# Kernel tuning notes

Hardware: AMD Instinct MI355X
Metric: run time of the kernel (lower is better)

The kernel has to match this reference:

```python
import jax, jax.numpy as jnp
import numpy as np
import math

D_MODEL = 512
N_HEADS = 8
D_FF = 2048
E_LAYERS = 2
ENC_IN = 3
MA_K = 25            # moving_avg kernel size
FACTOR = 1
B, L_CYC, CDL = 16, 20, 128
SEQ = L_CYC * CDL    # 2560
TOP_K = int(FACTOR * math.log(SEQ))  # 7
OUTPUT_NUM = 1


def moving_avg(x, k=MA_K):
    # x: [B,S,D]; replicate-pad ends by (k-1)//2, stride-1 mean pool -> length S
    p = (k - 1) // 2
    xp = jnp.concatenate([jnp.repeat(x[:, :1], p, axis=1), x, jnp.repeat(x[:, -1:], p, axis=1)], axis=1)
    c = jnp.cumsum(xp, axis=1)
    c = jnp.concatenate([jnp.zeros_like(c[:, :1]), c], axis=1)
    return (c[:, k:] - c[:, :-k]) / k


def token_embed(x, W):
    # x: [B,S,C], W: [D_MODEL, C, 3]; Conv1d k=3, circular padding, no bias
    xc = jnp.pad(x.transpose(0, 2, 1), ((0, 0), (0, 0), (1, 1)), mode='wrap')
    y = jax.lax.conv_general_dilated(xc, W, (1,), 'VALID', dimension_numbers=('NCH', 'OIH', 'NCH'))
    return y.transpose(0, 2, 1)  # [B,S,D]


def autocorrelation(q, k, v):
    # q,k,v: [B,S,H,E]; FFT autocorrelation + top-k time-delay aggregation (inference path)
    B_, S, H, E = q.shape
    qf = jnp.fft.rfft(q.transpose(0, 2, 3, 1), axis=-1)      # [B,H,E,F]
    kf = jnp.fft.rfft(k.transpose(0, 2, 3, 1), axis=-1)
    corr = jnp.fft.irfft(qf * jnp.conj(kf), n=S, axis=-1)    # [B,H,E,S]
    vals = v.transpose(0, 2, 3, 1)                           # [B,H,E,S]
    mean_corr = corr.mean(axis=(1, 2))                       # [B,S]
    weights, delay = jax.lax.top_k(mean_corr, TOP_K)         # [B,K]
    w = jax.nn.softmax(weights, axis=-1)

    def agg_one(v_b, d_b, w_b):
        # roll by -delay == gather values at index (t + delay) mod S
        out = jnp.zeros_like(v_b)
        for i in range(TOP_K):
            out = out + jnp.roll(v_b, -d_b[i], axis=-1) * w_b[i]
        return out

    V = jax.vmap(agg_one)(vals, delay, w)                    # [B,H,E,S]
    return V.transpose(0, 3, 1, 2)                           # [B,S,H,E]


def my_layernorm(x, g, b):
    # LayerNorm over last dim, then subtract the per-series (time) mean
    mu = x.mean(-1, keepdims=True)
    var = ((x - mu) ** 2).mean(-1, keepdims=True)
    xh = (x - mu) / jnp.sqrt(var + 1e-5) * g + b
    return xh - xh.mean(axis=1, keepdims=True)


def encoder_layer(x, Wq, bq, Wk, bk, Wv, bv, Wo, bo, Wc1, Wc2):
    B_, S, D = x.shape
    H, E = N_HEADS, D // N_HEADS
    q = (x @ Wq + bq).reshape(B_, S, H, E)
    k = (x @ Wk + bk).reshape(B_, S, H, E)
    v = (x @ Wv + bv).reshape(B_, S, H, E)
    att = autocorrelation(q, k, v).reshape(B_, S, D)
    x = x + (att @ Wo + bo)
    x = x - moving_avg(x)                                    # series_decomp1: residual part
    y = jax.nn.gelu(x @ Wc1, approximate=False) @ Wc2        # 1x1 convs, no bias
    z = x + y
    return z - moving_avg(z)                                 # series_decomp2


def setup_inputs() -> dict:
    key = jax.random.key(0)
    ks = jax.random.split(key, 12)
    s = 0.02
    rn = lambda k, shape: jax.random.normal(k, shape, dtype=jnp.float32) * s
    return {
        'cycle_curve_data': jax.random.normal(ks[0], (B, L_CYC, ENC_IN, CDL), dtype=jnp.float32),
        'curve_attn_mask': jnp.ones((B, L_CYC), dtype=jnp.float32),
        'W_emb': rn(ks[1], (D_MODEL, ENC_IN, 3)),
        'Wq': rn(ks[2], (E_LAYERS, D_MODEL, D_MODEL)),
        'bq': jnp.zeros((E_LAYERS, D_MODEL), jnp.float32),
        'Wk': rn(ks[3], (E_LAYERS, D_MODEL, D_MODEL)),
        'bk': jnp.zeros((E_LAYERS, D_MODEL), jnp.float32),
        'Wv': rn(ks[4], (E_LAYERS, D_MODEL, D_MODEL)),
        'bv': jnp.zeros((E_LAYERS, D_MODEL), jnp.float32),
        'Wo': rn(ks[5], (E_LAYERS, D_MODEL, D_MODEL)),
        'bo': jnp.zeros((E_LAYERS, D_MODEL), jnp.float32),
        'Wc1': rn(ks[6], (E_LAYERS, D_MODEL, D_FF)),
        'Wc2': rn(ks[7], (E_LAYERS, D_FF, D_MODEL)),
        'gamma': jnp.ones((D_MODEL,), jnp.float32),
        'beta': jnp.zeros((D_MODEL,), jnp.float32),
        'Wp': rn(ks[8], (D_MODEL * SEQ, OUTPUT_NUM)),
        'bp': jnp.zeros((OUTPUT_NUM,), jnp.float32),
    }


def reference(cycle_curve_data, curve_attn_mask, W_emb, Wq, bq, Wk, bk, Wv, bv, Wo, bo, Wc1, Wc2, gamma, beta, Wp, bp):
    mask = curve_attn_mask[:, :, None, None]                 # [B,L,1,1]
    x = jnp.where(mask == 0, 0.0, cycle_curve_data)          # zero masked cycles
    Bn = x.shape[0]
    x = x.transpose(0, 1, 3, 2).reshape(Bn, SEQ, ENC_IN)     # [B, L*CDL, NV]
    h = token_embed(x, W_emb)                                # DataEmbedding_wo_pos (x_mark=None, dropout=0)
    for l in range(E_LAYERS):
        h = encoder_layer(h, Wq[l], bq[l], Wk[l], bk[l], Wv[l], bv[l], Wo[l], bo[l], Wc1[l], Wc2[l])
    h = my_layernorm(h, gamma, beta)
    out = jax.nn.gelu(h, approximate=False)
    emb = out.reshape(Bn, -1)
    return emb @ Wp + bp                                     # [B, OUTPUT_NUM]
```

## Files before the change

### kernel.cpp

```cpp
#include <hip/hip_runtime.h>
#include <math.h>

#define BATCH 16
#define L_CYC 20
#define CDL 128
#define SEQ 2560
#define ENC_IN 3
#define DMODEL 512
#define DFF 2048
#define NLAYERS 2
#define TOPK 7
#define MROWS (BATCH*SEQ)
#define SD ((size_t)BATCH * SEQ * DMODEL)
#define FFN_CHUNK 20480
#define CHUNK_D 256
#define DGRP 8
#define FFT_NT 512

typedef short bf16x8 __attribute__((ext_vector_type(8)));
typedef float f32x4 __attribute__((ext_vector_type(4)));

__device__ __forceinline__ float gelu_f(float x) {
    float z = x * 0.70710678118654752f;
    float az = fabsf(z);
    float t = __builtin_amdgcn_rcpf(1.0f + 0.3275911f * az);
    float poly = t * (0.254829592f + t * (-0.284496736f + t * (1.421413741f
               + t * (-1.453152027f + t * 1.061405429f))));
    float e = __expf(-az * az);
    float erfv = 1.0f - poly * e;
    erfv = copysignf(erfv, z);
    return 0.5f * x * (1.0f + erfv);
}
__device__ __forceinline__ unsigned short f2bf(float f) {
    unsigned int u = __float_as_uint(f);
    u += 0x7fff + ((u >> 16) & 1);
    return (unsigned short)(u >> 16);
}
__device__ __forceinline__ float bf2f(unsigned short h) {
    return __uint_as_float(((unsigned int)h) << 16);
}
__device__ __forceinline__ void xcd_map(int p, int G, int& g, int& n) {
    int a = p >> 3;
    n = a % G;
    g = (a / G) * 8 + (p & 7);
}
__device__ __forceinline__ void gload16(const unsigned short* g, unsigned short* l) {
    typedef unsigned int u32;
    __builtin_amdgcn_global_load_lds(
        (const __attribute__((address_space(1))) u32*)g,
        (__attribute__((address_space(3))) u32*)l, 16, 0, 0);
}

__global__ __launch_bounds__(256) void embed_kernel(
    const float* __restrict__ data, const float* __restrict__ mask,
    const float* __restrict__ Wemb, float* __restrict__ h,
    unsigned short* __restrict__ hi, unsigned short* __restrict__ lo) {
    __shared__ float xv[2][9];
    int tid = threadIdx.x;
    size_t r0 = (size_t)blockIdx.x * 2;
    if (tid < 18) {
        int lr = tid / 9, k = tid % 9;
        int t = k / 3, c = k % 3;
        size_t r = r0 + lr;
        int s = (int)(r % SEQ);
        int b = (int)(r / SEQ);
        int u = s - 1 + t;
        if (u < 0) u += SEQ;
        if (u >= SEQ) u -= SEQ;
        int cyc = u >> 7, pos = u & 127;
        float mk = mask[b * L_CYC + cyc];
        xv[lr][c * 3 + t] = (mk == 0.f) ? 0.f
            : data[(((size_t)b * L_CYC + cyc) * ENC_IN + c) * CDL + pos];
    }
    __syncthreads();
    int lr = tid >> 7;
    int dm = (tid & 127) * 4;
    size_t idx = (r0 + lr) * DMODEL + dm;
    float a[4];
#pragma unroll
    for (int q = 0; q < 4; q++) {
        float acc = 0.f;
#pragma unroll
        for (int j = 0; j < 9; j++) acc += xv[lr][j] * Wemb[(dm + q) * 9 + j];
        a[q] = acc;
    }
    *(float4*)(h + idx) = make_float4(a[0], a[1], a[2], a[3]);
    ushort4 hv = make_ushort4(f2bf(a[0]), f2bf(a[1]), f2bf(a[2]), f2bf(a[3]));
    *(ushort4*)(hi + idx) = hv;
    ushort4 lv = make_ushort4(f2bf(a[0] - bf2f(hv.x)), f2bf(a[1] - bf2f(hv.y)),
                              f2bf(a[2] - bf2f(hv.z)), f2bf(a[3] - bf2f(hv.w)));
    *(ushort4*)(lo + idx) = lv;
}

__global__ __launch_bounds__(256) void transpose_bf16_kernel(
    const float* __restrict__ W, unsigned short* __restrict__ Wt, int K, int N) {
    __shared__ float t[32][33];
    int n0 = blockIdx.x * 32, k0 = blockIdx.y * 32;
    int c = threadIdx.x & 31, r = threadIdx.x >> 5;
    for (int i = 0; i < 4; i++)
        t[r + i * 8][c] = W[(size_t)(k0 + r + i * 8) * N + n0 + c];
    __syncthreads();
    for (int i = 0; i < 4; i++)
        Wt[(size_t)(n0 + r + i * 8) * K + k0 + c] = f2bf(t[c][r + i * 8]);
}

__global__ __launch_bounds__(256) void transpose_split_stk_kernel(
    const float* __restrict__ W, unsigned short* __restrict__ WtH,
    unsigned short* __restrict__ WtL, int which) {
    __shared__ float t[32][33];
    int n0 = blockIdx.x * 32, k0 = blockIdx.y * 32;
    int c = threadIdx.x & 31, r = threadIdx.x >> 5;
    for (int i = 0; i < 4; i++)
        t[r + i * 8][c] = W[(size_t)(k0 + r + i * 8) * DMODEL + n0 + c];
    __syncthreads();
    for (int i = 0; i < 4; i++) {
        int n = n0 + r + i * 8;
        int row = (n & 255) + ((n >> 8) * 512) + which * 256;
        float v = t[c][r + i * 8];
        unsigned short h = f2bf(v);
        size_t o = (size_t)row * DMODEL + k0 + c;
        WtH[o] = h;
        WtL[o] = f2bf(v - bf2f(h));
    }
}

__global__ void stack_bias_kernel(const float* __restrict__ bq,
                                  const float* __restrict__ bk, float* __restrict__ bstk) {
    int i = blockIdx.x * 256 + threadIdx.x;
    if (i >= 1024) return;
    int c = i >> 9, j = i & 511;
    bstk[i] = (j < 256) ? bq[c * 256 + j] : bk[c * 256 + (j - 256)];
}

__global__ __launch_bounds__(256) void wvo_kernel(
    const float* __restrict__ Wv, const float* __restrict__ Wo,
    float* __restrict__ Wvo) {
    __shared__ float row[DMODEL];
    int k = blockIdx.x;
    int tid = threadIdx.x;
    for (int j = tid; j < DMODEL; j += 256) row[j] = Wv[(size_t)k * DMODEL + j];
    __syncthreads();
    float a0 = 0.f, a1 = 0.f;
    for (int j = 0; j < DMODEL; j++) {
        float wv = row[j];
        a0 += wv * Wo[(size_t)j * DMODEL + tid];
        a1 += wv * Wo[(size_t)j * DMODEL + tid + 256];
    }
    Wvo[(size_t)k * DMODEL + tid] = a0;
    Wvo[(size_t)k * DMODEL + tid + 256] = a1;
}

__global__ void cbias_kernel(const float* __restrict__ bv, const float* __restrict__ Wo,
                             const float* __restrict__ bo, float* __restrict__ cb) {
    int n = blockIdx.x * 256 + threadIdx.x;
    if (n >= DMODEL) return;
    float acc = bo[n];
    for (int j = 0; j < DMODEL; j++) acc += bv[j] * Wo[(size_t)j * DMODEL + n];
    cb[n] = acc;
}

#define BK 64
__global__ __launch_bounds__(256) void gemm_mfma_kernel(
    const unsigned short* __restrict__ A, const unsigned short* __restrict__ Wt,
    const float* __restrict__ bias, const float* res,
    void* Cout, int M, int N, int K, int act, int outMode, int gridN)
{
    __shared__ unsigned short As[128 * 64];
    __shared__ unsigned short Bs[128 * 64];
    int tid = threadIdx.x;
    int wave = tid >> 6, lane = tid & 63;
    int wm = wave & 1, wn = wave >> 1;
    int gblk, nblk;
    xcd_map(blockIdx.x, gridN, gblk, nblk);
    int bm = gblk * 128, bn = nblk * 128;

    int r8 = lane >> 3;
    int swc = ((lane & 7) ^ r8) * 8;
    const unsigned short* Agb = A  + (size_t)(bm + wave * 32 + r8) * K + swc;
    const unsigned short* Bgb = Wt + (size_t)(bn + wave * 32 + r8) * K + swc;
    unsigned short* AsW = As + wave * 32 * 64;
    unsigned short* BsW = Bs + wave * 32 * 64;

    f32x4 acc[4][4] = {};
    int frow = lane & 15;
    int fj = lane >> 4;
    int s7 = frow & 7;

    for (int k0 = 0; k0 < K; k0 += BK) {
        __syncthreads();
#pragma unroll
        for (int i = 0; i < 4; i++) {
            gload16(Agb + (size_t)(i * 8) * K + k0, AsW + i * 8 * 64);
            gload16(Bgb + (size_t)(i * 8) * K + k0, BsW + i * 8 * 64);
        }
        asm volatile("s_waitcnt vmcnt(0)" ::: "memory");
        __syncthreads();
#pragma unroll
        for (int kk = 0; kk < 2; kk++) {
            int c16 = (((kk << 2) | fj) ^ s7) << 3;
            bf16x8 af[4], bfv[4];
#pragma unroll
            for (int mi = 0; mi < 4; mi++)
                af[mi] = *(const bf16x8*)&As[(wm * 64 + mi * 16 + frow) * 64 + c16];
#pragma unroll
            for (int nj = 0; nj < 4; nj++)
                bfv[nj] = *(const bf16x8*)&Bs[(wn * 64 + nj * 16 + frow) * 64 + c16];
#pragma unroll
            for (int mi = 0; mi < 4; mi++)
#pragma unroll
                for (int nj = 0; nj < 4; nj++)
                    acc[mi][nj] = __builtin_amdgcn_mfma_f32_16x16x32_bf16(
                        af[mi], bfv[nj], acc[mi][nj], 0, 0, 0);
        }
    }

    int lrow = (lane >> 4) * 4, lcol = lane & 15;
#pragma unroll
    for (int mi = 0; mi < 4; mi++) {
        int row0 = bm + wm * 64 + mi * 16 + lrow;
#pragma unroll
        for (int nj = 0; nj < 4; nj++) {
            int col = bn + wn * 64 + nj * 16 + lcol;
            float bv = bias ? bias[col] : 0.f;
            f32x4 v = acc[mi][nj];
#pragma unroll
            for (int r = 0; r < 4; r++) {
                int row = row0 + r;
                float x = v[r] + bv;
                if (res) x += res[(size_t)row * N + col];
                if (act == 1) x = gelu_f(x);
                if (outMode == 0) ((float*)Cout)[(size_t)row * N + col] = x;
                else              ((unsigned short*)Cout)[(size_t)row * N + col] = f2bf(x);
            }
        }
    }
}

#define QBK 32
__global__ __launch_bounds__(256) void gemm_qk_split_kernel(
    const unsigned short* __restrict__ Ahi, const unsigned short* __restrict__ Alo,
    const unsigned short* __restrict__ Whi, const unsigned short* __restrict__ Wlo,
    const float* __restrict__ bias, float* __restrict__ Ct, int M, int K, int gridN)
{
    __shared__ unsigned short AsH[128 * 32];
    __shared__ unsigned short AsL[128 * 32];
    __shared__ unsigned short BsH[128 * 32];
    __shared__ unsigned short BsL[128 * 32];
    int tid = threadIdx.x;
    int wave = tid >> 6, lane = tid & 63;
    int wm = wave & 1, wn = wave >> 1;
    int gblk, nblk;
    xcd_map(blockIdx.x, gridN, gblk, nblk);
    int bm = gblk * 128, bn = nblk * 128;

    int lrs = lane >> 2;
    int lk  = (((lane & 3) ^ ((lane >> 3) & 3))) * 8;

    f32x4 acc[4][4] = {};
    int frow = lane & 15;
    int fk = (((lane >> 4) ^ ((frow >> 1) & 3))) * 8;

    for (int k0 = 0; k0 < K; k0 += QBK) {
        __syncthreads();
#pragma unroll
        for (int i = 0; i < 2; i++) {
            int j = wave * 2 + i;
            int row = j * 16 + lrs;
            size_t oa = (size_t)(bm + row) * K + k0 + lk;
            size_t ob = (size_t)(bn + row) * K + k0 + lk;
            gload16(Ahi + oa, AsH + j * 512);
            gload16(Alo + oa, AsL + j * 512);
            gload16(Whi + ob, BsH + j * 512);
            gload16(Wlo + ob, BsL + j * 512);
        }
        asm volatile("s_waitcnt vmcnt(0)" ::: "memory");
        __syncthreads();
        bf16x8 afh[4], afl[4], bfh[4], bfl[4];
#pragma unroll
        for (int mi = 0; mi < 4; mi++) {
            int o = (wm * 64 + mi * 16 + frow) * 32 + fk;
            afh[mi] = *(const bf16x8*)&AsH[o];
            afl[mi] = *(const bf16x8*)&AsL[o];
        }
#pragma unroll
        for (int nj = 0; nj < 4; nj++) {
            int o = (wn * 64 + nj * 16 + frow) * 32 + fk;
            bfh[nj] = *(const bf16x8*)&BsH[o];
            bfl[nj] = *(const bf16x8*)&BsL[o];
        }
#pragma unroll
        for (int mi = 0; mi < 4; mi++)
#pragma unroll
            for (int nj = 0; nj < 4; nj++) {
                acc[mi][nj] = __builtin_amdgcn_mfma_f32_16x16x32_bf16(
                    afh[mi], bfh[nj], acc[mi][nj], 0, 0, 0);
                acc[mi][nj] = __builtin_amdgcn_mfma_f32_16x16x32_bf16(
                    afh[mi], bfl[nj], acc[mi][nj], 0, 0, 0);
                acc[mi][nj] = __builtin_amdgcn_mfma_f32_16x16x32_bf16(
                    afl[mi], bfh[nj], acc[mi][nj], 0, 0, 0);
            }
    }

    int lrow = (lane >> 4) * 4, lcol = lane & 15;
#pragma unroll
    for (int mi = 0; mi < 4; mi++) {
        int row0 = bm + wm * 64 + mi * 16 + lrow;
#pragma unroll
        for (int nj = 0; nj < 4; nj++) {
            int col = bn + wn * 64 + nj * 16 + lcol;
            float bv = bias ? bias[col] : 0.f;
            f32x4 v = acc[mi][nj];
#pragma unroll
            for (int r = 0; r < 4; r++)
                Ct[(size_t)col * M + row0 + r] = v[r] + bv;
        }
    }
}

__device__ __forceinline__ int swz(int a) { return a ^ ((a >> 4) & 15); }

template<int LOGS, int NT>
__device__ __forceinline__ void radix4_stage(const float2* __restrict__ X,
                                             float2* __restrict__ Y,
                                             const float2* __restrict__ w512x,
                                             int tid) {
    const int s = 1 << LOGS;
    for (int t = tid; t < 640; t += NT) {
        int sub = t >> 7, r = t & 127;
        int base = sub << 9;
        int q = r & (s - 1);
        int ps = r - q;
        float2 x0 = X[swz(base + r)];
        float2 x1 = X[swz(base + r + 128)];
        float2 x2 = X[swz(base + r + 256)];
        float2 x3 = X[swz(base + r + 384)];
        float A0r = x0.x + x2.x, A0i = x0.y + x2.y;
        float B0r = x1.x + x3.x, B0i = x1.y + x3.y;
        float A1r = x0.x - x2.x, A1i = x0.y - x2.y;
        float B1r = x1.x - x3.x, B1i = x1.y - x3.y;
        float2 w1 = w512x[ps];
        float w2r = w1.x * w1.x - w1.y * w1.y;
        float w2i = 2.0f * w1.x * w1.y;
        float w3r = w2r * w1.x - w2i * w1.y;
        float w3i = w2r * w1.y + w2i * w1.x;
        float u1r = A1r + B1i, u1i = A1i - B1r;
        float u2r = A0r - B0r, u2i = A0i - B0i;
        float u3r = A1r - B1i, u3i = A1i + B1r;
        int ob = base + q + 4 * ps;
        Y[swz(ob)]         = make_float2(A0r + B0r, A0i + B0i);
        Y[swz(ob + s)]     = make_float2(u1r * w1.x - u1i * w1.y,
                                         u1r * w1.y + u1i * w1.x);
        Y[swz(ob + 2 * s)] = make_float2(u2r * w2r - u2i * w2i,
                                         u2r * w2i + u2i * w2r);
        Y[swz(ob + 3 * s)] = make_float2(u3r * w3r - u3i * w3i,
                                         u3r * w3i + u3i * w3r);
    }
}

template<int NT>
__device__ void fft2560(const float2* x, float2* bufA, float2* bufB,
                        const float2* w512x, const float2* tw, int tid) {
    {
        const float w5r[5] = { 1.f,  0.30901699437494742f, -0.80901699437494742f,
                              -0.80901699437494742f,  0.30901699437494742f };
        const float w5i[5] = { 0.f, -0.95105651629515357f, -0.58778525229247312f,
                               0.58778525229247312f,  0.95105651629515357f };
#pragma unroll
        for (int k1 = 0; k1 < 5; k1++) {
            float ar = 0.f, ai = 0.f;
#pragma unroll
            for (int n1 = 0; n1 < 5; n1++) {
                int m = (n1 * k1) % 5;
                ar += x[n1].x * w5r[m] - x[n1].y * w5i[m];
                ai += x[n1].x * w5i[m] + x[n1].y * w5r[m];
            }
            if (k1 == 0) {
                bufB[swz(tid)] = make_float2(ar, ai);
            } else {
                float2 w = tw[k1 - 1];
                bufB[swz(k1 * 512 + tid)] =
                    make_float2(ar * w.x - ai * w.y, ar * w.y + ai * w.x);
            }
        }
    }
    __syncthreads();
    radix4_stage<0, NT>(bufB, bufA, w512x, tid); __syncthreads();
    radix4_stage<2, NT>(bufA, bufB, w512x, tid); __syncthreads();
    radix4_stage<4, NT>(bufB, bufA, w512x, tid); __syncthreads();
    radix4_stage<6, NT>(bufA, bufB, w512x, tid); __syncthreads();
    for (int t = tid; t < 1280; t += NT) {
        int sub = t >> 8, q = t & 255;
        int base = sub << 9;
        float2 a = bufB[swz(base + q)];
        float2 b = bufB[swz(base + q + 256)];
        bufA[swz(base + q)]       = make_float2(a.x + b.x, a.y + b.y);
        bufA[swz(base + q + 256)] = make_float2(a.x - b.x, a.y - b.y);
    }
    __syncthreads();
}

__global__ __launch_bounds__(FFT_NT) void fft_fwd_kernel(
    const float* __restrict__ qt, const float* __restrict__ kt, float* __restrict__ Z)
{
    __shared__ float2 bufA[SEQ];
    __shared__ float2 bufB[SEQ];
    __shared__ float2 w512x[512];
    int d0 = blockIdx.x * DGRP;
    int b = blockIdx.y;
    int tid = threadIdx.x;
    {
        float sn, cs;
        sincosf(-6.283185307179586f * (float)tid / 512.0f, &sn, &cs);
        w512x[tid] = make_float2(cs, sn);
    }
    float2 tw[4];
#pragma unroll
    for (int k1 = 1; k1 <= 4; k1++) {
        float sn, cs;
        sincosf(-2.4543692606170259e-3f * (float)(k1 * tid), &sn, &cs);
        tw[k1 - 1] = make_float2(cs, sn);
    }
    float accR[5], accI[5];
#pragma unroll
    for (int j = 0; j < 5; j++) { accR[j] = 0.f; accI[j] = 0.f; }

    for (int col = 0; col < DGRP; col++) {
        const float* qcol = qt + (size_t)(d0 + col) * MROWS + (size_t)b * SEQ;
        const float* kcol = kt + (size_t)(d0 + col) * MROWS + (size_t)b * SEQ;
        float2 x[5];
#pragma unroll
        for (int m = 0; m < 5; m++)
            x[m] = make_float2(qcol[m * 512 + tid], kcol[m * 512 + tid]);
        fft2560<FFT_NT>(x, bufA, bufB, w512x, tw, tid);
#pragma unroll
        for (int j = 0; j < 5; j++) {
            int f = tid + FFT_NT * j;
            int fpos = (f % 5) * 512 + (f / 5);
            int g = f ? (SEQ - f) : 0;
            int gpos = (g % 5) * 512 + (g / 5);
            float2 Z1 = bufA[swz(fpos)], Z2 = bufA[swz(gpos)];
            accR[j] += 0.5f * (Z1.x * Z2.y + Z1.y * Z2.x);
            accI[j] += 0.25f * ((Z1.x * Z1.x + Z1.y * Z1.y)
                              - (Z2.x * Z2.x + Z2.y * Z2.y));
        }
    }
#pragma unroll
    for (int j = 0; j < 5; j++) {
        int f = tid + FFT_NT * j;
        int fpos = (f % 5) * 512 + (f / 5);
        atomicAdd(&Z[((size_t)b * SEQ + fpos) * 2 + 0], accR[j]);
        atomicAdd(&Z[((size_t)b * SEQ + fpos) * 2 + 1], accI[j]);
    }
}

__global__ __launch_bounds__(FFT_NT) void fft_inv_kernel(
    const float* __restrict__ Z, float* __restrict__ mc)
{
    __shared__ float2 bufA[SEQ];
    __shared__ float2 bufB[SEQ];
    __shared__ float2 w512x[512];
    int b = blockIdx.x;
    int tid = threadIdx.x;
    {
        float sn, cs;
        sincosf(-6.283185307179586f * (float)tid / 512.0f, &sn, &cs);
        w512x[tid] = make_float2(cs, sn);
    }
    float2 tw[4];
#pragma unroll
    for (int k1 = 1; k1 <= 4; k1++) {
        float sn, cs;
        sincosf(-2.4543692606170259e-3f * (float)(k1 * tid), &sn, &cs);
        tw[k1 - 1] = make_float2(cs, sn);
    }
    float2 x[5];
#pragma unroll
    for (int m = 0; m < 5; m++) {
        int i = m * 512 + tid;
        int k1 = i % 5, k2 = i / 5;
        float zr = Z[((size_t)b * SEQ + k1 * 512 + k2) * 2 + 0];
        float zi = Z[((size_t)b * SEQ + k1 * 512 + k2) * 2 + 1];
        x[m] = make_float2(zr, -zi);
    }
    fft2560<FFT_NT>(x, bufA, bufB, w512x, tw, tid);
    const float scale = 1.0f / (2560.0f * 512.0f);
    for (int j = tid; j < SEQ; j += FFT_NT) {
        int k1 = j >> 9, k2 = j & 511;
        mc[(size_t)b * SEQ + k1 + 5 * k2] = bufA[swz(j)].x * scale;
    }
}

__global__ __launch_bounds__(256) void topk_kernel(
    const float* __restrict__ mc, float* __restrict__ wts, int* __restrict__ dels)
{
    __shared__ float cv[SEQ];
    __shared__ float rv[256];
    __shared__ int   ri[256];
    __shared__ float topv[TOPK];
    __shared__ int   topi[TOPK];
    int b = blockIdx.x, tid = threadIdx.x;
    for (int i = tid; i < SEQ; i += 256) cv[i] = mc[(size_t)b * SEQ + i];
    __syncthreads();
    for (int it = 0; it < TOPK; it++) {
        float bv = -2e30f; int bi = 1 << 30;
        for (int i = tid; i < SEQ; i += 256) {
            float v = cv[i];
            if (v > bv || (v == bv && i < bi)) { bv = v; bi = i; }
        }
        rv[tid] = bv; ri[tid] = bi;
        __syncthreads();
        for (int off = 128; off > 0; off >>= 1) {
            if (tid < off) {
                float v2 = rv[tid + off]; int i2 = ri[tid + off];
                if (v2 > rv[tid] || (v2 == rv[tid] && i2 < ri[tid])) {
                    rv[tid] = v2; ri[tid] = i2;
                }
            }
            __syncthreads();
        }
        if (tid == 0) { topv[it] = rv[0]; topi[it] = ri[0]; cv[ri[0]] = -1e30f; }
        __syncthreads();
    }
    if (tid == 0) {
        float mx = topv[0];
        float e[TOPK], ssum = 0.f;
        for (int i = 0; i < TOPK; i++) { e[i] = expf(topv[i] - mx); ssum += e[i]; }
        for (int i = 0; i < TOPK; i++) {
            wts[b * TOPK + i] = e[i] / ssum;
            dels[b * TOPK + i] = topi[i];
        }
    }
}

__global__ void agg_res_kernel(const float* __restrict__ u, const float* __restrict__ x,
                               const float* __restrict__ cb,
                               const float* __restrict__ wts, const int* __restrict__ dels,
                               float* __restrict__ x1) {
    size_t i4 = ((size_t)blockIdx.x * 256 + threadIdx.x) * 4;
    if (i4 >= SD) return;
    int d = (int)(i4 & (DMODEL - 1));
    size_t r = i4 >> 9;
    int s = (int)(r % SEQ);
    int b = (int)(r / SEQ);
    float4 xx = *(const float4*)(x + i4);
    float4 cc = *(const float4*)(cb + d);
    float a0 = cc.x + xx.x, a1 = cc.y + xx.y, a2 = cc.z + xx.z, a3 = cc.w + xx.w;
    const float* ub = u + (size_t)b * SEQ * DMODEL + d;
#pragma unroll
    for (int i = 0; i < TOPK; i++) {
        int del = dels[b * TOPK + i];
        float w = wts[b * TOPK + i];
        int ss = s + del; if (ss >= SEQ) ss -= SEQ;
        float4 uu = *(const float4*)(ub + (size_t)ss * DMODEL);
        a0 += w * uu.x; a1 += w * uu.y; a2 += w * uu.z; a3 += w * uu.w;
    }
    *(float4*)(x1 + i4) = make_float4(a0, a1, a2, a3);
}

#define MA_MODE_PLAIN 0
#define MA_MODE_BF    1
#define MA_MODE_SPLIT 2
template<int MODE>
__device__ __forceinline__ void ma_run_body(
    const float* __restrict__ x, float* __restrict__ out,
    unsigned short* __restrict__ o1, unsigned short* __restrict__ o2)
{
    int tid = threadIdx.x;
    int s0 = blockIdx.x * 128;
    int d  = blockIdx.y * 256 + tid;
    int b  = blockIdx.z;
    const float* xb = x + (size_t)b * SEQ * DMODEL + d;
    float sum = 0.f;
#pragma unroll
    for (int j = -12; j <= 12; j++) {
        int ss = s0 + j;
        ss = ss < 0 ? 0 : (ss > SEQ - 1 ? SEQ - 1 : ss);
        sum += xb[(size_t)ss * DMODEL];
    }
    for (int s = s0; s < s0 + 128; s++) {
        float v = xb[(size_t)s * DMODEL] - sum * (1.0f / 25.0f);
        size_t o = ((size_t)b * SEQ + s) * DMODEL + d;
        out[o] = v;
        if (MODE == MA_MODE_BF) {
            o1[o] = f2bf(v);
        } else if (MODE == MA_MODE_SPLIT) {
            unsigned short h = f2bf(v);
            o1[o] = h;
            o2[o] = f2bf(v - bf2f(h));
        }
        int add = s + 13; if (add > SEQ - 1) add = SEQ - 1;
        int sub = s - 12; if (sub < 0) sub = 0;
        sum += xb[(size_t)add * DMODEL] - xb[(size_t)sub * DMODEL];
    }
}
__global__ __launch_bounds__(256) void ma_sub_kernel(
    const float* __restrict__ x, float* __restrict__ out) {
    ma_run_body<MA_MODE_PLAIN>(x, out, nullptr, nullptr);
}
__global__ __launch_bounds__(256) void ma_sub_bf_kernel(
    const float* __restrict__ x, float* __restrict__ out,
    unsigned short* __restrict__ obf) {
    ma_run_body<MA_MODE_BF>(x, out, obf, nullptr);
}
__global__ __launch_bounds__(256) void ma_sub_split_kernel(
    const float* __restrict__ x, float* __restrict__ out,
    unsigned short* __restrict__ hi, unsigned short* __restrict__ lo) {
    ma_run_body<MA_MODE_SPLIT>(x, out, hi, lo);
}

__global__ __launch_bounds__(256) void ln_kernel(
    const float* __restrict__ x, const float* __restrict__ g,
    const float* __restrict__ be, float* __restrict__ xh)
{
    int row = blockIdx.x;
    int tid = threadIdx.x;
    __shared__ float red[256];
    const float* xr = x + (size_t)row * DMODEL;
    float v0 = xr[tid], v1 = xr[tid + 256];
    red[tid] = v0 + v1;
    __syncthreads();
    for (int off = 128; off > 0; off >>= 1) {
        if (tid < off) red[tid] += red[tid + off];
        __syncthreads();
    }
    float mu = red[0] / (float)DMODEL;
    __syncthreads();
    float d0 = v0 - mu, d1 = v1 - mu;
    red[tid] = d0 * d0 + d1 * d1;
    __syncthreads();
    for (int off = 128; off > 0; off >>= 1) {
        if (tid < off) red[tid] += red[tid + off];
        __syncthreads();
    }
    float inv = rsqrtf(red[0] / (float)DMODEL + 1e-5f);
    xh[(size_t)row * DMODEL + tid]       = d0 * inv * g[tid] + be[tid];
    xh[(size_t)row * DMODEL + tid + 256] = d1 * inv * g[tid + 256] + be[tid + 256];
}

__global__ __launch_bounds__(256) void colmean_kernel(
    const float* __restrict__ xh, float* __restrict__ cm) {
    int q = blockIdx.x * 256 + threadIdx.x;
    int idx = q * 4;
    int d = idx & (DMODEL - 1), b = idx >> 9;
    int s0 = blockIdx.y * 128;
    const float* xb = xh + (size_t)b * SEQ * DMODEL + d;
    float a0 = 0.f, a1 = 0.f, a2 = 0.f, a3 = 0.f;
    for (int s = s0; s < s0 + 128; s++) {
        float4 v = *(const float4*)(xb + (size_t)s * DMODEL);
        a0 += v.x; a1 += v.y; a2 += v.z; a3 += v.w;
    }
    atomicAdd(&cm[idx + 0], a0 * (1.0f / (float)SEQ));
    atomicAdd(&cm[idx + 1], a1 * (1.0f / (float)SEQ));
    atomicAdd(&cm[idx + 2], a2 * (1.0f / (float)SEQ));
    atomicAdd(&cm[idx + 3], a3 * (1.0f / (float)SEQ));
}

__global__ __launch_bounds__(256) void final_kernel(
    const float* __restrict__ xh, const float* __restrict__ cm,
    const float* __restrict__ Wp, const float* __restrict__ bp,
    float* __restrict__ out)
{
    int b = blockIdx.y, chunk = blockIdx.x;
    int tid = threadIdx.x;
    const size_t per = (size_t)SEQ * DMODEL / 64;
    size_t start = (size_t)chunk * per;
    float acc = 0.f;
    for (size_t i = start + tid * 4; i < start + per; i += 1024) {
        int d = (int)(i & (DMODEL - 1));
        float4 v = *(const float4*)(xh + (size_t)b * SEQ * DMODEL + i);
        float4 c = *(const float4*)(cm + b * DMODEL + d);
        float4 w = *(const float4*)(Wp + i);
        acc += gelu_f(v.x - c.x) * w.x + gelu_f(v.y - c.y) * w.y
             + gelu_f(v.z - c.z) * w.z + gelu_f(v.w - c.w) * w.w;
    }
    __shared__ float red[256];
    red[tid] = acc;
    __syncthreads();
    for (int off = 128; off > 0; off >>= 1) {
        if (tid < off) red[tid] += red[tid + off];
        __syncthreads();
    }
    if (tid == 0) {
        atomicAdd(&out[b], red[0]);
        if (chunk == 0) atomicAdd(&out[b], bp[0]);
    }
}

extern "C" void kernel_launch(void* const* d_in, const int* in_sizes, int n_in,
                              void* d_out, int out_size, void* d_ws, size_t ws_size,
                              hipStream_t stream) {
    const float* data  = (const float*)d_in[0];
    const float* mask  = (const float*)d_in[1];
    const float* Wemb  = (const float*)d_in[2];
    const float* Wq    = (const float*)d_in[3];
    const float* bq    = (const float*)d_in[4];
    const float* Wk    = (const float*)d_in[5];
    const float* bk    = (const float*)d_in[6];
    const float* Wv    = (const float*)d_in[7];
    const float* bv    = (const float*)d_in[8];
    const float* Wo    = (const float*)d_in[9];
    const float* bo    = (const float*)d_in[10];
    const float* Wc1   = (const float*)d_in[11];
    const float* Wc2   = (const float*)d_in[12];
    const float* gamma = (const float*)d_in[13];
    const float* beta  = (const float*)d_in[14];
    const float* Wp    = (const float*)d_in[15];
    const float* bp    = (const float*)d_in[16];
    float* out = (float*)d_out;

    float* buf0 = (float*)d_ws;
    float* buf1 = buf0 + SD;
    float* buf2 = buf1 + SD;

    unsigned short* WstkH = (unsigned short*)(buf2 + SD);
    unsigned short* WstkL = WstkH + 2 * DMODEL * DMODEL;
    unsigned short* Wvot  = WstkL + 2 * DMODEL * DMODEL;
    unsigned short* Wc1t  = Wvot + DMODEL * DMODEL;
    unsigned short* Wc2t  = Wc1t + (size_t)DMODEL * DFF;
    float* WvoF = (float*)(Wc2t + (size_t)DMODEL * DFF);
    float* CB   = WvoF + (size_t)DMODEL * DMODEL;
    float* Bstk = CB + DMODEL;
    float* Zb = Bstk + 1024;
    float* MC = Zb + (size_t)BATCH * SEQ * 2;
    float* WT = MC + (size_t)BATCH * SEQ;
    int*   DL = (int*)(WT + BATCH * TOPK);
    float* CM = (float*)(DL + BATCH * TOPK);

    const int NB  = (int)((SD + 255) / 256);
    const int NB4 = (int)((SD / 4 + 255) / 256);
    dim3 gMA(SEQ / 128, 2, BATCH);

    float* X  = buf0;
    float* HL = buf1;
    float* S  = buf2;

    embed_kernel<<<MROWS / 2, 256, 0, stream>>>(data, mask, Wemb, X,
                                                (unsigned short*)HL + SD,
                                                (unsigned short*)HL);

    const int gSqBlocks = (MROWS / 128) * (DMODEL / 128);
    const int gF1Blocks = (FFN_CHUNK / 128) * (DFF / 128);
    const int gF2Blocks = (FFN_CHUNK / 128) * (DMODEL / 128);

    for (int l = 0; l < NLAYERS; l++) {
        const float* wq = Wq + (size_t)l * DMODEL * DMODEL;
        const float* wk = Wk + (size_t)l * DMODEL * DMODEL;
        const float* wv = Wv + (size_t)l * DMODEL * DMODEL;
        const float* wo = Wo + (size_t)l * DMODEL * DMODEL;
        const float* bqL = bq + (size_t)l * DMODEL;
        const float* bkL = bk + (size_t)l * DMODEL;
        const float* bvL = bv + (size_t)l * DMODEL;
        const float* boL = bo + (size_t)l * DMODEL;
        const float* wc1 = Wc1 + (size_t)l * DMODEL * DFF;
        const float* wc2 = Wc2 + (size_t)l * DFF * DMODEL;

        unsigned short* Lbf = (unsigned short*)HL;
        unsigned short* Hbf = Lbf + SD;
        float* qtf = S;
        float* ktf = S + (size_t)MROWS * CHUNK_D;

        dim3 gT(DMODEL / 32, DMODEL / 32);
        transpose_split_stk_kernel<<<gT, 256, 0, stream>>>(wq, WstkH, WstkL, 0);
        transpose_split_stk_kernel<<<gT, 256, 0, stream>>>(wk, WstkH, WstkL, 1);
        stack_bias_kernel<<<4, 256, 0, stream>>>(bqL, bkL, Bstk);
        wvo_kernel<<<DMODEL, 256, 0, stream>>>(wv, wo, WvoF);
        transpose_bf16_kernel<<<gT, 256, 0, stream>>>(WvoF, Wvot, DMODEL, DMODEL);
        cbias_kernel<<<2, 256, 0, stream>>>(bvL, wo, boL, CB);
        transpose_bf16_kernel<<<dim3(DFF / 32, DMODEL / 32), 256, 0, stream>>>(wc1, Wc1t, DMODEL, DFF);
        transpose_bf16_kernel<<<dim3(DMODEL / 32, DFF / 32), 256, 0, stream>>>(wc2, Wc2t, DFF, DMODEL);

        hipMemsetAsync(Zb, 0, (size_t)BATCH * SEQ * 2 * sizeof(float), stream);
        for (int c = 0; c < DMODEL / CHUNK_D; c++) {
            gemm_qk_split_kernel<<<gSqBlocks, 256, 0, stream>>>(
                Hbf, Lbf, WstkH + (size_t)c * 512 * DMODEL,
                WstkL + (size_t)c * 512 * DMODEL, Bstk + c * 512,
                S, MROWS, DMODEL, DMODEL / 128);
            fft_fwd_kernel<<<dim3(CHUNK_D / DGRP, BATCH), FFT_NT, 0, stream>>>(qtf, ktf, Zb);
        }
        fft_inv_kernel<<<BATCH, FFT_NT, 0, stream>>>(Zb, MC);
        topk_kernel<<<BATCH, 256, 0, stream>>>(MC, WT, DL);

        gemm_mfma_kernel<<<gSqBlocks, 256, 0, stream>>>(Hbf, Wvot, nullptr, nullptr, S,
                                                        MROWS, DMODEL, DMODEL, 0, 0,
                                                        DMODEL / 128);
        agg_res_kernel<<<NB4, 256, 0, stream>>>(S, X, CB, WT, DL, HL);
        ma_sub_bf_kernel<<<gMA, 256, 0, stream>>>(HL, X, (unsigned short*)S);
        for (int c = 0; c < MROWS / FFN_CHUNK; c++) {
            const unsigned short* x2c = (unsigned short*)S + (size_t)c * FFN_CHUNK * DMODEL;
            float* xz = X + (size_t)c * FFN_CHUNK * DMODEL;
            gemm_mfma_kernel<<<gF1Blocks, 256, 0, stream>>>(x2c, Wc1t, nullptr, nullptr,
                                                            (unsigned short*)HL,
                                                            FFN_CHUNK, DFF, DMODEL, 1, 1,
                                                            DFF / 128);
            gemm_mfma_kernel<<<gF2Blocks, 256, 0, stream>>>((unsigned short*)HL, Wc2t,
                                                            nullptr, xz, xz,
                                                            FFN_CHUNK, DMODEL, DFF, 0, 0,
                                                            DMODEL / 128);
        }
        if (l + 1 < NLAYERS)
            ma_sub_split_kernel<<<gMA, 256, 0, stream>>>(
                X, S, (unsigned short*)HL + SD, (unsigned short*)HL);
        else
            ma_sub_kernel<<<gMA, 256, 0, stream>>>(X, S);
        float* tmp = X; X = S; S = tmp;
    }

    ln_kernel<<<MROWS, 256, 0, stream>>>(X, gamma, beta, HL);
    hipMemsetAsync(CM, 0, (size_t)BATCH * DMODEL * sizeof(float), stream);
    colmean_kernel<<<dim3(8, 20), 256, 0, stream>>>(HL, CM);
    hipMemsetAsync(out, 0, (size_t)out_size * sizeof(float), stream);
    final_kernel<<<dim3(64, BATCH), 256, 0, stream>>>(HL, CM, Wp, bp, out);
}
```

Before: 1.984 ms.

## Double-buffer LDS tiles in MFMA GEMM with BK=32 and prefetch overlap

The bf16 MFMA GEMM now keeps two LDS buffers of 32-wide K tiles. It issues the global-to-LDS loads for the next tile after reading fragments from the current one, so the loads overlap the MFMA work. This removes one barrier per iteration and hides global load latency. In exchange, K steps are half as large, so there are twice as many iterations, each still waiting on vmcnt(0) and a barrier, and the new swizzle pattern may change LDS bank conflicts.

```diff
diff --git a/kernel.cpp b/kernel.cpp
--- a/kernel.cpp
+++ b/kernel.cpp
@@ -159,14 +159,14 @@
     cb[n] = acc;
 }
 
-#define BK 64
+#define BK 32
 __global__ __launch_bounds__(256) void gemm_mfma_kernel(
     const unsigned short* __restrict__ A, const unsigned short* __restrict__ Wt,
     const float* __restrict__ bias, const float* res,
     void* Cout, int M, int N, int K, int act, int outMode, int gridN)
 {
-    __shared__ unsigned short As[128 * 64];
-    __shared__ unsigned short Bs[128 * 64];
+    __shared__ unsigned short As[2][128 * 32];
+    __shared__ unsigned short Bs[2][128 * 32];
     int tid = threadIdx.x;
     int wave = tid >> 6, lane = tid & 63;
     int wm = wave & 1, wn = wave >> 1;
@@ -174,44 +174,51 @@
     xcd_map(blockIdx.x, gridN, gblk, nblk);
     int bm = gblk * 128, bn = nblk * 128;
 
-    int r8 = lane >> 3;
-    int swc = ((lane & 7) ^ r8) * 8;
-    const unsigned short* Agb = A  + (size_t)(bm + wave * 32 + r8) * K + swc;
-    const unsigned short* Bgb = Wt + (size_t)(bn + wave * 32 + r8) * K + swc;
-    unsigned short* AsW = As + wave * 32 * 64;
-    unsigned short* BsW = Bs + wave * 32 * 64;
+    int lrs = lane >> 2;
+    int lk  = (((lane & 3) ^ ((lane >> 3) & 3))) * 8;
+    int j0 = wave * 2, j1 = wave * 2 + 1;
+    const unsigned short* Ag0 = A  + (size_t)(bm + j0 * 16 + lrs) * K + lk;
+    const unsigned short* Ag1 = A  + (size_t)(bm + j1 * 16 + lrs) * K + lk;
+    const unsigned short* Bg0 = Wt + (size_t)(bn + j0 * 16 + lrs) * K + lk;
+    const unsigned short* Bg1 = Wt + (size_t)(bn + j1 * 16 + lrs) * K + lk;
 
     f32x4 acc[4][4] = {};
     int frow = lane & 15;
-    int fj = lane >> 4;
-    int s7 = frow & 7;
-
-    for (int k0 = 0; k0 < K; k0 += BK) {
-        __syncthreads();
-#pragma unroll
-        for (int i = 0; i < 4; i++) {
-            gload16(Agb + (size_t)(i * 8) * K + k0, AsW + i * 8 * 64);
-            gload16(Bgb + (size_t)(i * 8) * K + k0, BsW + i * 8 * 64);
-        }
+    int fk = (((lane >> 4) ^ ((frow >> 1) & 3))) * 8;
+    int nst = K / BK;
+
+    gload16(Ag0, &As[0][j0 * 512]);
+    gload16(Ag1, &As[0][j1 * 512]);
+    gload16(Bg0, &Bs[0][j0 * 512]);
+    gload16(Bg1, &Bs[0][j1 * 512]);
+    asm volatile("s_waitcnt vmcnt(0)" ::: "memory");
+    __syncthreads();
+
+    for (int t = 0; t < nst; ++t) {
+        int cur = t & 1, nxt = cur ^ 1;
+        bf16x8 af[4], bfv[4];
+#pragma unroll
+        for (int mi = 0; mi < 4; mi++)
+            af[mi] = *(const bf16x8*)&As[cur][(wm * 64 + mi * 16 + frow) * 32 + fk];
+#pragma unroll
+        for (int nj = 0; nj < 4; nj++)
+            bfv[nj] = *(const bf16x8*)&Bs[cur][(wn * 64 + nj * 16 + frow) * 32 + fk];
+        __builtin_amdgcn_sched_barrier(0);
+        if (t + 1 < nst) {
+            int k0 = (t + 1) * BK;
+            gload16(Ag0 + k0, &As[nxt][j0 * 512]);
+            gload16(Ag1 + k0, &As[nxt][j1 * 512]);
+            gload16(Bg0 + k0, &Bs[nxt][j0 * 512]);
+            gload16(Bg1 + k0, &Bs[nxt][j1 * 512]);
+        }
+#pragma unroll
+        for (int mi = 0; mi < 4; mi++)
+#pragma unroll
+            for (int nj = 0; nj < 4; nj++)
+                acc[mi][nj] = __builtin_amdgcn_mfma_f32_16x16x32_bf16(
+                    af[mi], bfv[nj], acc[mi][nj], 0, 0, 0);
         asm volatile("s_waitcnt vmcnt(0)" ::: "memory");
         __syncthreads();
-#pragma unroll
-        for (int kk = 0; kk < 2; kk++) {
-            int c16 = (((kk << 2) | fj) ^ s7) << 3;
-            bf16x8 af[4], bfv[4];
-#pragma unroll
-            for (int mi = 0; mi < 4; mi++)
-                af[mi] = *(const bf16x8*)&As[(wm * 64 + mi * 16 + frow) * 64 + c16];
-#pragma unroll
-            for (int nj = 0; nj < 4; nj++)
-                bfv[nj] = *(const bf16x8*)&Bs[(wn * 64 + nj * 16 + frow) * 64 + c16];
-#pragma unroll
-            for (int mi = 0; mi < 4; mi++)
-#pragma unroll
-                for (int nj = 0; nj < 4; nj++)
-                    acc[mi][nj] = __builtin_amdgcn_mfma_f32_16x16x32_bf16(
-                        af[mi], bfv[nj], acc[mi][nj], 0, 0, 0);
-        }
     }
 
     int lrow = (lane >> 4) * 4, lcol = lane & 15;
```

New measurement: 1.959 ms. No clear change (-1.3%).
